# Optimization experiments

Hardware: AMD Instinct MI355X
Metric: run time of the kernel (lower is better)

The kernel has to match this reference:

```python
import jax, jax.numpy as jnp
import numpy as np

B, N, K, DIN, DM, DOUT = 4, 8192, 16, 128, 128, 128
SCALE = 1.0 / float(np.sqrt(DM))


def setup_inputs() -> dict:
    key = jax.random.key(0)
    ks = jax.random.split(key, 24)
    s = 0.05
    rnd = lambda k, shape: jax.random.normal(k, shape, jnp.float32) * s
    return {
        "relative_knn_xyz": jax.random.normal(ks[0], (B, N, K, 3), jnp.float32),
        "feature": jax.random.normal(ks[1], (B, N, DIN), jnp.float32),
        "knn_idx": jax.random.randint(ks[2], (B, N, K), 0, N),
        # fc_delta: Linear(3,DM) -> ReLU -> Linear(DM,DM)
        "Wd1": rnd(ks[3], (3, DM)), "bd1": jnp.zeros((DM,), jnp.float32),
        "Wd2": rnd(ks[4], (DM, DM)), "bd2": jnp.zeros((DM,), jnp.float32),
        # fc1: Linear(DIN, DM)
        "W1": rnd(ks[5], (DIN, DM)), "b1": jnp.zeros((DM,), jnp.float32),
        # q/k/v projections (no bias)
        "Wq": rnd(ks[6], (DM, DM)),
        "Wk": rnd(ks[7], (DM, DM)),
        "Wv": rnd(ks[8], (DM, DM)),
        # fc_gamma: Linear(DM,DM) -> ReLU -> Linear(DM,DM)
        "Wg1": rnd(ks[9], (DM, DM)), "bg1": jnp.zeros((DM,), jnp.float32),
        "Wg2": rnd(ks[10], (DM, DM)), "bg2": jnp.zeros((DM,), jnp.float32),
        # fc2: Linear(DM, DOUT)
        "W2": rnd(ks[11], (DM, DOUT)), "b2": jnp.zeros((DOUT,), jnp.float32),
        # shortout_fc: Linear(DIN, DOUT)
        "Ws": rnd(ks[12], (DIN, DOUT)), "bs": jnp.zeros((DOUT,), jnp.float32),
    }


def reference(relative_knn_xyz, feature, knn_idx,
              Wd1, bd1, Wd2, bd2, W1, b1, Wq, Wk, Wv,
              Wg1, bg1, Wg2, bg2, W2, b2, Ws, bs):
    # positional encoding of relative knn coords: [B,N,K,DM]
    pos_enc = jax.nn.relu(relative_knn_xyz @ Wd1 + bd1) @ Wd2 + bd2
    f = feature @ W1 + b1                                  # [B,N,DM]
    bidx = jnp.arange(B)[:, None, None]
    knn_f = f[bidx, knn_idx]                               # gather -> [B,N,K,DM]
    q = f @ Wq                                             # [B,N,DM]
    k = knn_f @ Wk                                         # [B,N,K,DM]
    v = knn_f @ Wv                                         # [B,N,K,DM]
    h = q[:, :, None, :] - k + pos_enc                     # [B,N,K,DM]
    logits = (jax.nn.relu(h @ Wg1 + bg1) @ Wg2 + bg2) * SCALE
    attn = jax.nn.softmax(logits, axis=-2)                 # softmax over neighbors
    agg = jnp.einsum('bnkf,bnkf->bnf', attn, v + pos_enc)  # [B,N,DM]
    return agg @ W2 + b2 + feature @ Ws + bs               # [B,N,DOUT]
```

## Files before the change

kernel.cpp:

```cpp
#include <hip/hip_runtime.h>

#define NB 4
#define NN 8192
#define NK 16
#define ND 128
#define NPTS (NB*NN)

typedef __bf16 bv8 __attribute__((ext_vector_type(8)));
typedef unsigned short us8 __attribute__((ext_vector_type(8)));
typedef float fv4 __attribute__((ext_vector_type(4)));
typedef float f32x16 __attribute__((ext_vector_type(16)));
typedef unsigned int u32;

__device__ __forceinline__ unsigned short f2b(float x){
  union { float f; unsigned u; } v; v.f = x;
  unsigned r = v.u + 0x7FFFu + ((v.u >> 16) & 1u);
  return (unsigned short)(r >> 16);
}
__device__ __forceinline__ float blo(u32 u){ return __builtin_bit_cast(float, u << 16); }
__device__ __forceinline__ float bhi(u32 u){ return __builtin_bit_cast(float, u & 0xffff0000u); }
__device__ __forceinline__ u32 pkbf(float lo, float hi){
  u32 r; asm("v_cvt_pk_bf16_f32 %0, %1, %2" : "=v"(r) : "v"(lo), "v"(hi)); return r;
}
__device__ __forceinline__ unsigned swz(int row, int cbyte){
  return (unsigned)(row*256 + (cbyte ^ ((row & 7) << 4)));
}
__device__ __forceinline__ unsigned aggoff(int pt, int c16){
  return (unsigned)(pt*128 + (c16 ^ ((pt & 7) << 3)));
}
__device__ __forceinline__ fv4 mfma16(us8 a, us8 b, fv4 c){
  return __builtin_amdgcn_mfma_f32_16x16x32_bf16(
      __builtin_bit_cast(bv8, a), __builtin_bit_cast(bv8, b), c, 0, 0, 0);
}
__device__ __forceinline__ f32x16 mfma32(us8 a, us8 b, f32x16 c){
  return __builtin_amdgcn_mfma_f32_32x32x16_bf16(
      __builtin_bit_cast(bv8, a), __builtin_bit_cast(bv8, b), c, 0, 0, 0);
}
__device__ __forceinline__ us8 mkb(u32 w0, u32 w1, u32 w2, u32 w3){
  union { u32 w[4]; us8 v; } u; u.w[0]=w0; u.w[1]=w1; u.w[2]=w2; u.w[3]=w3; return u.v;
}
__device__ __forceinline__ f32x16 zf(){
  f32x16 z;
  #pragma unroll
  for (int i=0;i<16;++i) z[i]=0.f;
  return z;
}
__device__ __forceinline__ float rsum16(float v){
  v += __builtin_bit_cast(float, __builtin_amdgcn_update_dpp(0, __builtin_bit_cast(int, v), 0x128, 0xf, 0xf, false));
  v += __builtin_bit_cast(float, __builtin_amdgcn_update_dpp(0, __builtin_bit_cast(int, v), 0x124, 0xf, 0xf, false));
  v += __builtin_bit_cast(float, __builtin_amdgcn_update_dpp(0, __builtin_bit_cast(int, v), 0x122, 0xf, 0xf, false));
  v += __builtin_bit_cast(float, __builtin_amdgcn_update_dpp(0, __builtin_bit_cast(int, v), 0x121, 0xf, 0xf, false));
  return v;
}

__global__ void pt_prep1(const float* __restrict__ Wk, const float* __restrict__ Wq,
                         const float* __restrict__ Wg1, float* __restrict__ T1, float* __restrict__ T2){
  int b = blockIdx.x;
  const float* A = (b >= 4) ? Wq : Wk;
  float* D = (b >= 4) ? T2 : T1;
  int row = (b & 3)*32 + (threadIdx.x >> 3);
  int c0 = (threadIdx.x & 7)*16;
  float acc[16];
  #pragma unroll
  for (int j=0;j<16;++j) acc[j]=0.f;
  for (int k=0;k<128;++k){
    float a = A[row*128+k];
    const float* g = Wg1 + k*128 + c0;
    #pragma unroll
    for (int j=0;j<16;++j) acc[j] = fmaf(a, g[j], acc[j]);
  }
  #pragma unroll
  for (int j=0;j<16;++j) D[row*128 + c0 + j] = acc[j];
}

__global__ void pt_prep2(const float* __restrict__ W1, const float* __restrict__ Wv,
                         const float* __restrict__ Wd2, const float* __restrict__ Wg1,
                         const float* __restrict__ T1, const float* __restrict__ T2,
                         const float* __restrict__ b1, const float* __restrict__ bd2,
                         const float* __restrict__ bg1, const float* __restrict__ b2,
                         const float* __restrict__ W2,
                         float* __restrict__ WKG, float* __restrict__ WQG,
                         float* __restrict__ WV, float* __restrict__ W21,
                         float* __restrict__ bKG, float* __restrict__ bQG,
                         float* __restrict__ bV, float* __restrict__ b2p)
{
  int b = blockIdx.x;
  if (b < 16){
    int pr = b >> 2;
    const float* A  = (pr==3) ? Wd2 : W1;
    const float* Bm = (pr==0) ? T1 : (pr==1) ? T2 : (pr==2) ? Wv : Wg1;
    float* D        = (pr==0) ? WKG : (pr==1) ? WQG : (pr==2) ? WV : W21;
    int row = (b & 3)*32 + (threadIdx.x >> 3);
    int c0 = (threadIdx.x & 7)*16;
    float acc[16];
    #pragma unroll
    for (int j=0;j<16;++j) acc[j]=0.f;
    for (int k=0;k<128;++k){
      float a = A[row*128+k];
      const float* g = Bm + k*128 + c0;
      #pragma unroll
      for (int j=0;j<16;++j) acc[j] = fmaf(a, g[j], acc[j]);
    }
    #pragma unroll
    for (int j=0;j<16;++j) D[row*128 + c0 + j] = acc[j];
  } else if (threadIdx.x < 128){
    int j = threadIdx.x;
    float s1=0.f, s2=0.f, s3=0.f, s4=0.f;
    for (int k=0;k<128;++k){
      s1 = fmaf(b1[k],  T1[k*128+j],  s1);
      s2 = fmaf(b1[k],  T2[k*128+j],  s2);
      s2 = fmaf(bd2[k], Wg1[k*128+j], s2);
      s3 = fmaf(b1[k],  Wv[k*128+j],  s3);
      s4 = fmaf(bd2[k], W2[k*128+j],  s4);
    }
    bKG[j] = s1;
    bQG[j] = s2 + bg1[j];
    bV[j]  = s3;
    b2p[j] = b2[j] + s4;
  }
}

__global__ void pt_pack(const float* __restrict__ WKG, const float* __restrict__ WQG,
                        const float* __restrict__ WV, const float* __restrict__ Ws,
                        const float* __restrict__ W21, const float* __restrict__ Wd2,
                        const float* __restrict__ Wg2, const float* __restrict__ W2,
                        const float* __restrict__ Wd1, const float* __restrict__ bd1,
                        unsigned short* __restrict__ pstd, unsigned short* __restrict__ pT,
                        unsigned short* __restrict__ pD1)
{
  int b = blockIdx.x;
  if (b < 4){
    const float* srcs[4] = {WKG, WQG, WV, Ws};
    const float* src = srcs[b];
    unsigned short* dst = pstd + b*16384;
    for (int e = threadIdx.x; e < 16384; e += blockDim.x){
      int j = e&7, lane = (e>>3)&63, ct = (e>>9)&7, kb = (e>>12)&3;
      int row = kb*32 + ((lane>>4)<<3) + j;
      int col = ct*16 + (lane&15);
      dst[e] = f2b(src[row*128+col]);
    }
  } else if (b < 8){
    const float* srcs[4] = {W21, Wd2, Wg2, W2};
    const float* src = srcs[b-4];
    unsigned short* dst = pT + (b-4)*16384;
    for (int e = threadIdx.x; e < 16384; e += blockDim.x){
      int j = e&7, lane = (e>>3)&63, kb = (e>>9)&7, mt = (e>>12)&3;
      int row = mt*32 + (lane&31);
      int k = kb*16 + ((lane>>5)<<3) + j;
      dst[e] = f2b(src[k*128+row]);
    }
  } else {
    for (int e = threadIdx.x; e < 2048; e += blockDim.x){
      int j = e&7, lane = (e>>3)&63, mt = (e>>9)&3;
      int c = mt*32 + (lane&31);
      int k = ((lane>>5)<<3) + j;
      float v = (k<3) ? Wd1[k*128+c] : ((k==3) ? bd1[c] : 0.f);
      pD1[e] = f2b(v);
    }
  }
}

__global__ __launch_bounds__(256) void pt_proj(
    const float* __restrict__ feat, const unsigned short* __restrict__ pstd,
    const float* __restrict__ bKG, const float* __restrict__ bQG,
    const float* __restrict__ bV, const float* __restrict__ bs,
    unsigned short* __restrict__ KG, unsigned short* __restrict__ QG,
    unsigned short* __restrict__ Vv, float* __restrict__ SH)
{
  __shared__ alignas(16) char ldsF[32768];
  int tid = threadIdx.x;
  int bid = blockIdx.x;
  int panel = bid & 3;
  int rb = (bid >> 2) * 128;
  {
    int rr = tid>>1, c0 = (tid&1)*64;
    const float* src = feat + (rb+rr)*128 + c0;
    #pragma unroll
    for (int c=0;c<64;c+=4){
      float4 v = *(const float4*)(src + c);
      u32 w0 = (u32)f2b(v.x) | ((u32)f2b(v.y)<<16);
      u32 w1 = (u32)f2b(v.z) | ((u32)f2b(v.w)<<16);
      *(uint2*)(ldsF + swz(rr, (c0+c)*2)) = make_uint2(w0,w1);
    }
  }
  __syncthreads();
  int w = tid>>6, l = tid&63;
  int row0 = w*32;
  int arow = l&15, acb = (l>>4)<<4;
  int crw = (l>>4)<<2, ccol = l&15;
  const unsigned short* Bp = pstd + panel*16384;
  fv4 acc[2][8];
  #pragma unroll
  for (int rt=0;rt<2;++rt)
    #pragma unroll
    for (int ct=0;ct<8;++ct) acc[rt][ct] = fv4{0.f,0.f,0.f,0.f};
  #pragma unroll
  for (int kb=0;kb<4;++kb){
    us8 a0 = *(const us8*)(ldsF + swz(row0+arow,    kb*64+acb));
    us8 a1 = *(const us8*)(ldsF + swz(row0+16+arow, kb*64+acb));
    #pragma unroll
    for (int ct=0;ct<8;++ct){
      us8 bf = *(const us8*)(Bp + ((kb*8+ct)*64 + l)*8);
      acc[0][ct] = mfma16(a0, bf, acc[0][ct]);
      acc[1][ct] = mfma16(a1, bf, acc[1][ct]);
    }
  }
  const float* bias = (panel==0)?bKG:(panel==1)?bQG:(panel==2)?bV:bs;
  if (panel < 3){
    unsigned short* dst = (panel==0)?KG:(panel==1)?QG:Vv;
    #pragma unroll
    for (int rt=0;rt<2;++rt)
      #pragma unroll
      for (int ct=0;ct<8;++ct)
        #pragma unroll
        for (int rg=0;rg<4;++rg){
          int r = row0 + rt*16 + crw + rg, c = ct*16 + ccol;
          dst[(rb+r)*128 + c] = f2b(acc[rt][ct][rg] + bias[c]);
        }
  } else {
    #pragma unroll
    for (int rt=0;rt<2;++rt)
      #pragma unroll
      for (int ct=0;ct<8;++ct)
        #pragma unroll
        for (int rg=0;rg<4;++rg){
          int r = row0 + rt*16 + crw + rg, c = ct*16 + ccol;
          SH[(rb+r)*128 + c] = acc[rt][ct][rg] + bias[c];
        }
  }
}

__global__ __launch_bounds__(512, 2) void pt_main(
    const int* __restrict__ knn, const float* __restrict__ xyz,
    const unsigned short* __restrict__ KG, const unsigned short* __restrict__ QG,
    const unsigned short* __restrict__ Vv, const float* __restrict__ SH,
    const unsigned short* __restrict__ pT, const unsigned short* __restrict__ pD1,
    const float* __restrict__ b2p, float* __restrict__ outp)
{
  __shared__ unsigned short aggL[32*128];
  const unsigned short* pW21T = pT + 0*16384;
  const unsigned short* pWd2T = pT + 1*16384;
  const unsigned short* pWg2T = pT + 2*16384;
  const unsigned short* pW2T  = pT + 3*16384;

  int tid = threadIdx.x;
  int bid = blockIdx.x;
  int wgx = (bid & 7)*256 + (bid >> 3);
  int gp0 = wgx * 16;
  int bb  = gp0 >> 13;
  int w = tid >> 6, l = tid & 63;
  int h = l >> 5, r = l & 31, p = r >> 4, n = r & 15;
  int mypt = gp0 + w*2 + p;
  int ptl  = w*2 + p;

  ((unsigned long long*)aggL)[512 + tid] = 0ull;

  int gidx = (bb << 13) + knn[mypt*16 + n];
  const float* xr = xyz + (mypt*16 + n)*3;
  float xx = xr[0], xy = xr[1], xz = xr[2];

  u32 bx0 = h ? 0u : pkbf(xx, xy);
  u32 bx1 = h ? 0u : pkbf(xz, 1.0f);
  us8 bX = mkb(bx0, bx1, 0u, 0u);
  f32x16 P1f[4];
  #pragma unroll
  for (int mt=0; mt<4; ++mt){
    us8 aW = *(const us8*)(pD1 + (mt*64 + l)*8);
    P1f[mt] = mfma32(aW, bX, zf());
  }
  u32 pw[4][4][2];
  #pragma unroll
  for (int mt=0; mt<4; ++mt)
    #pragma unroll
    for (int q=0; q<4; ++q)
      #pragma unroll
      for (int wi=0; wi<2; ++wi)
        pw[mt][q][wi] = pkbf(fmaxf(0.f, P1f[mt][4*q+2*wi]),
                             fmaxf(0.f, P1f[mt][4*q+2*wi+1]));

  u32 Bp[8][4];
  #pragma unroll
  for (int kb=0; kb<8; ++kb){
    int ms = kb>>1, qA = 2*(kb&1), qB = qA+1;
    u32 sA0 = __shfl_xor(pw[ms][qA][0], 32), sA1 = __shfl_xor(pw[ms][qA][1], 32);
    u32 sB0 = __shfl_xor(pw[ms][qB][0], 32), sB1 = __shfl_xor(pw[ms][qB][1], 32);
    Bp[kb][0] = h ? sB0 : pw[ms][qA][0];
    Bp[kb][1] = h ? sB1 : pw[ms][qA][1];
    Bp[kb][2] = h ? pw[ms][qB][0] : sA0;
    Bp[kb][3] = h ? pw[ms][qB][1] : sA1;
  }

  uint2 kg[4][4], qg[4][4];
  {
    const unsigned short* kgr = KG + gidx*128;
    const unsigned short* qgr = QG + mypt*128;
    #pragma unroll
    for (int mt=0; mt<4; ++mt)
      #pragma unroll
      for (int q=0; q<4; ++q){
        kg[mt][q] = *(const uint2*)(kgr + 32*mt + 8*q + 4*h);
        qg[mt][q] = *(const uint2*)(qgr + 32*mt + 8*q + 4*h);
      }
  }

  f32x16 pg[4];
  #pragma unroll
  for (int mt=0; mt<4; ++mt) pg[mt] = zf();
  #pragma unroll
  for (int kb=0; kb<8; ++kb){
    us8 bfr = mkb(Bp[kb][0], Bp[kb][1], Bp[kb][2], Bp[kb][3]);
    #pragma unroll
    for (int mt=0; mt<4; ++mt){
      us8 a = *(const us8*)(pW21T + ((mt*8+kb)*64 + l)*8);
      pg[mt] = mfma32(a, bfr, pg[mt]);
    }
  }

  u32 gw[4][4][2];
  #pragma unroll
  for (int mt=0; mt<4; ++mt)
    #pragma unroll
    for (int q=0; q<4; ++q){
      float g0 = fmaxf(0.f, pg[mt][4*q+0] + (blo(qg[mt][q].x) - blo(kg[mt][q].x)));
      float g1 = fmaxf(0.f, pg[mt][4*q+1] + (bhi(qg[mt][q].x) - bhi(kg[mt][q].x)));
      float g2 = fmaxf(0.f, pg[mt][4*q+2] + (blo(qg[mt][q].y) - blo(kg[mt][q].y)));
      float g3 = fmaxf(0.f, pg[mt][4*q+3] + (bhi(qg[mt][q].y) - bhi(kg[mt][q].y)));
      gw[mt][q][0] = pkbf(g0, g1);
      gw[mt][q][1] = pkbf(g2, g3);
    }
  u32 Bg[8][4];
  #pragma unroll
  for (int kb=0; kb<8; ++kb){
    int ms = kb>>1, qA = 2*(kb&1), qB = qA+1;
    u32 sA0 = __shfl_xor(gw[ms][qA][0], 32), sA1 = __shfl_xor(gw[ms][qA][1], 32);
    u32 sB0 = __shfl_xor(gw[ms][qB][0], 32), sB1 = __shfl_xor(gw[ms][qB][1], 32);
    Bg[kb][0] = h ? sB0 : gw[ms][qA][0];
    Bg[kb][1] = h ? sB1 : gw[ms][qA][1];
    Bg[kb][2] = h ? gw[ms][qB][0] : sA0;
    Bg[kb][3] = h ? gw[ms][qB][1] : sA1;
  }

  uint2 vv[4][4];
  {
    const unsigned short* vr = Vv + gidx*128;
    #pragma unroll
    for (int mt=0; mt<4; ++mt)
      #pragma unroll
      for (int q=0; q<4; ++q)
        vv[mt][q] = *(const uint2*)(vr + 32*mt + 8*q + 4*h);
  }

  f32x16 lg[4];
  #pragma unroll
  for (int mt=0; mt<4; ++mt) lg[mt] = zf();
  #pragma unroll
  for (int kb=0; kb<8; ++kb){
    us8 bfr = mkb(Bg[kb][0], Bg[kb][1], Bg[kb][2], Bg[kb][3]);
    #pragma unroll
    for (int mt=0; mt<4; ++mt){
      us8 a = *(const us8*)(pWg2T + ((mt*8+kb)*64 + l)*8);
      lg[mt] = mfma32(a, bfr, lg[mt]);
    }
  }

  const float SC = 0.08838834764831843f;
  #pragma unroll
  for (int mt=0; mt<4; ++mt){
    f32x16 ps = zf();
    #pragma unroll
    for (int kb=0; kb<8; ++kb){
      us8 a = *(const us8*)(pWd2T + ((mt*8+kb)*64 + l)*8);
      ps = mfma32(a, mkb(Bp[kb][0], Bp[kb][1], Bp[kb][2], Bp[kb][3]), ps);
    }
    float aggv[16];
    #pragma unroll
    for (int q=0; q<4; ++q){
      float wv0 = blo(vv[mt][q].x) + ps[4*q+0];
      float wv1 = bhi(vv[mt][q].x) + ps[4*q+1];
      float wv2 = blo(vv[mt][q].y) + ps[4*q+2];
      float wv3 = bhi(vv[mt][q].y) + ps[4*q+3];
      float e0 = __expf(lg[mt][4*q+0]*SC);
      float e1 = __expf(lg[mt][4*q+1]*SC);
      float e2 = __expf(lg[mt][4*q+2]*SC);
      float e3 = __expf(lg[mt][4*q+3]*SC);
      float s0 = rsum16(e0), s1 = rsum16(e1), s2 = rsum16(e2), s3 = rsum16(e3);
      float m0 = rsum16(e0*wv0), m1 = rsum16(e1*wv1), m2 = rsum16(e2*wv2), m3 = rsum16(e3*wv3);
      aggv[4*q+0] = m0 * __builtin_amdgcn_rcpf(s0);
      aggv[4*q+1] = m1 * __builtin_amdgcn_rcpf(s1);
      aggv[4*q+2] = m2 * __builtin_amdgcn_rcpf(s2);
      aggv[4*q+3] = m3 * __builtin_amdgcn_rcpf(s3);
    }
    if ((l & 15) == 15){
      #pragma unroll
      for (int q=0; q<4; ++q){
        u32 w0 = pkbf(aggv[4*q+0], aggv[4*q+1]);
        u32 w1 = pkbf(aggv[4*q+2], aggv[4*q+3]);
        *(uint2*)(aggL + aggoff(ptl, 32*mt + 8*q + 4*h)) = make_uint2(w0, w1);
      }
    }
  }
  __syncthreads();

  if (w < 4){
    int mt = w;
    f32x16 o = zf();
    #pragma unroll
    for (int kb=0; kb<8; ++kb){
      us8 a = *(const us8*)(pW2T + ((mt*8+kb)*64 + l)*8);
      us8 bfr = *(const us8*)(aggL + aggoff(l&31, kb*16 + 8*h));
      o = mfma32(a, bfr, o);
    }
    int pt = l & 31;
    if (pt < 16){
      float* orow = outp + (gp0 + pt)*128;
      const float* shrow = SH + (gp0 + pt)*128;
      #pragma unroll
      for (int q=0; q<4; ++q){
        int cb = 32*mt + 8*q + 4*h;
        float4 b4 = *(const float4*)(b2p + cb);
        float4 s4 = *(const float4*)(shrow + cb);
        float4 res;
        res.x = o[4*q+0] + b4.x + s4.x;
        res.y = o[4*q+1] + b4.y + s4.y;
        res.z = o[4*q+2] + b4.z + s4.z;
        res.w = o[4*q+3] + b4.w + s4.w;
        *(float4*)(orow + cb) = res;
      }
    }
  }
}

extern "C" void kernel_launch(void* const* d_in, const int* in_sizes, int n_in,
                              void* d_out, int out_size, void* d_ws, size_t ws_size,
                              hipStream_t stream)
{
  const float* xyz     = (const float*)d_in[0];
  const float* feature = (const float*)d_in[1];
  const int*   knn     = (const int*)d_in[2];
  const float* Wd1 = (const float*)d_in[3];
  const float* bd1 = (const float*)d_in[4];
  const float* Wd2 = (const float*)d_in[5];
  const float* bd2 = (const float*)d_in[6];
  const float* W1  = (const float*)d_in[7];
  const float* b1  = (const float*)d_in[8];
  const float* Wq  = (const float*)d_in[9];
  const float* Wk  = (const float*)d_in[10];
  const float* Wv  = (const float*)d_in[11];
  const float* Wg1 = (const float*)d_in[12];
  const float* bg1 = (const float*)d_in[13];
  const float* Wg2 = (const float*)d_in[14];
  const float* bg2 = (const float*)d_in[15];
  const float* W2  = (const float*)d_in[16];
  const float* b2  = (const float*)d_in[17];
  const float* Ws  = (const float*)d_in[18];
  const float* bs  = (const float*)d_in[19];
  (void)bg2;

  char* ws = (char*)d_ws;
  unsigned short* KGa  = (unsigned short*)(ws + 0);
  unsigned short* QGa  = (unsigned short*)(ws + 8388608);
  unsigned short* Va   = (unsigned short*)(ws + 16777216);
  float*          SHa  = (float*)(ws + 25165824);
  unsigned short* PSTD = (unsigned short*)(ws + 41943040);
  unsigned short* PT   = (unsigned short*)(ws + 42074112);
  unsigned short* PD1  = (unsigned short*)(ws + 42205184);
  float* T1   = (float*)(ws + 42209280);
  float* T2   = (float*)(ws + 42274816);
  float* WKGf = (float*)(ws + 42340352);
  float* WQGf = (float*)(ws + 42405888);
  float* WVf  = (float*)(ws + 42471424);
  float* W21f = (float*)(ws + 42536960);
  float* bKG  = (float*)(ws + 42602496);
  float* bQG  = (float*)(ws + 42603008);
  float* bV   = (float*)(ws + 42603520);
  float* b2p  = (float*)(ws + 42604032);

  pt_prep1<<<8, 256, 0, stream>>>(Wk, Wq, Wg1, T1, T2);
  pt_prep2<<<17, 256, 0, stream>>>(W1, Wv, Wd2, Wg1, T1, T2, b1, bd2, bg1, b2, W2,
                                   WKGf, WQGf, WVf, W21f, bKG, bQG, bV, b2p);
  pt_pack<<<9, 256, 0, stream>>>(WKGf, WQGf, WVf, Ws, W21f, Wd2, Wg2, W2, Wd1, bd1,
                                 PSTD, PT, PD1);
  pt_proj<<<1024, 256, 0, stream>>>(feature, PSTD, bKG, bQG, bV, bs, KGa, QGa, Va, SHa);
  pt_main<<<2048, 512, 0, stream>>>(knn, xyz, KGa, QGa, Va, SHa, PT, PD1, b2p, (float*)d_out);
}
```

Measured before the change: 363.1 us.

## Fold q/k/v row adds into MFMA via identity matrices and use permlane32 swaps

The q-minus-k and v row additions move into the MFMA accumulators through extra MFMAs with ±identity A operands, in place of per-element bf16 unpacking and scalar adds. Gathered rows are loaded as 16-byte vectors, and the half-wave shuffles become v_permlane32_swap. The softmax scale and log2(e) are folded into Wg2 at pack time so exp2 can be used directly, and the small prep GEMMs are register-tiled with float4 loads. This adds MFMA work and identity-operand registers in exchange for fewer VALU and shuffle instructions.

Measured after the change: 306.5 us. 15.6% less time.

```diff
diff --git a/kernel.cpp b/kernel.cpp
--- a/kernel.cpp
+++ b/kernel.cpp
@@ -17,8 +17,6 @@
   unsigned r = v.u + 0x7FFFu + ((v.u >> 16) & 1u);
   return (unsigned short)(r >> 16);
 }
-__device__ __forceinline__ float blo(u32 u){ return __builtin_bit_cast(float, u << 16); }
-__device__ __forceinline__ float bhi(u32 u){ return __builtin_bit_cast(float, u & 0xffff0000u); }
 __device__ __forceinline__ u32 pkbf(float lo, float hi){
   u32 r; asm("v_cvt_pk_bf16_f32 %0, %1, %2" : "=v"(r) : "v"(lo), "v"(hi)); return r;
 }
@@ -52,25 +50,39 @@
   v += __builtin_bit_cast(float, __builtin_amdgcn_update_dpp(0, __builtin_bit_cast(int, v), 0x121, 0xf, 0xf, false));
   return v;
 }
+__device__ __forceinline__ void plswap(u32& a, u32& b){
+  asm("v_permlane32_swap_b32 %0, %1" : "+v"(a), "+v"(b));
+}
 
 __global__ void pt_prep1(const float* __restrict__ Wk, const float* __restrict__ Wq,
                          const float* __restrict__ Wg1, float* __restrict__ T1, float* __restrict__ T2){
   int b = blockIdx.x;
   const float* A = (b >= 4) ? Wq : Wk;
   float* D = (b >= 4) ? T2 : T1;
-  int row = (b & 3)*32 + (threadIdx.x >> 3);
-  int c0 = (threadIdx.x & 7)*16;
-  float acc[16];
-  #pragma unroll
-  for (int j=0;j<16;++j) acc[j]=0.f;
-  for (int k=0;k<128;++k){
-    float a = A[row*128+k];
-    const float* g = Wg1 + k*128 + c0;
-    #pragma unroll
-    for (int j=0;j<16;++j) acc[j] = fmaf(a, g[j], acc[j]);
-  }
-  #pragma unroll
-  for (int j=0;j<16;++j) D[row*128 + c0 + j] = acc[j];
+  int r0 = (b & 3)*32 + (threadIdx.x >> 5)*4;
+  int c0 = (threadIdx.x & 31)*4;
+  float4 acc[4];
+  #pragma unroll
+  for (int i=0;i<4;++i) acc[i] = make_float4(0.f,0.f,0.f,0.f);
+  for (int k = 0; k < 128; k += 4){
+    float4 a[4];
+    #pragma unroll
+    for (int i=0;i<4;++i) a[i] = *(const float4*)(A + (r0+i)*128 + k);
+    #pragma unroll
+    for (int kk=0; kk<4; ++kk){
+      float4 bv = *(const float4*)(Wg1 + (k+kk)*128 + c0);
+      #pragma unroll
+      for (int i=0;i<4;++i){
+        float av = (kk==0)?a[i].x:(kk==1)?a[i].y:(kk==2)?a[i].z:a[i].w;
+        acc[i].x = fmaf(av, bv.x, acc[i].x);
+        acc[i].y = fmaf(av, bv.y, acc[i].y);
+        acc[i].z = fmaf(av, bv.z, acc[i].z);
+        acc[i].w = fmaf(av, bv.w, acc[i].w);
+      }
+    }
+  }
+  #pragma unroll
+  for (int i=0;i<4;++i) *(float4*)(D + (r0+i)*128 + c0) = acc[i];
 }
 
 __global__ void pt_prep2(const float* __restrict__ W1, const float* __restrict__ Wv,
@@ -90,19 +102,30 @@
     const float* A  = (pr==3) ? Wd2 : W1;
     const float* Bm = (pr==0) ? T1 : (pr==1) ? T2 : (pr==2) ? Wv : Wg1;
     float* D        = (pr==0) ? WKG : (pr==1) ? WQG : (pr==2) ? WV : W21;
-    int row = (b & 3)*32 + (threadIdx.x >> 3);
-    int c0 = (threadIdx.x & 7)*16;
-    float acc[16];
-    #pragma unroll
-    for (int j=0;j<16;++j) acc[j]=0.f;
-    for (int k=0;k<128;++k){
-      float a = A[row*128+k];
-      const float* g = Bm + k*128 + c0;
-      #pragma unroll
-      for (int j=0;j<16;++j) acc[j] = fmaf(a, g[j], acc[j]);
-    }
-    #pragma unroll
-    for (int j=0;j<16;++j) D[row*128 + c0 + j] = acc[j];
+    int r0 = (b & 3)*32 + (threadIdx.x >> 5)*4;
+    int c0 = (threadIdx.x & 31)*4;
+    float4 acc[4];
+    #pragma unroll
+    for (int i=0;i<4;++i) acc[i] = make_float4(0.f,0.f,0.f,0.f);
+    for (int k = 0; k < 128; k += 4){
+      float4 a[4];
+      #pragma unroll
+      for (int i=0;i<4;++i) a[i] = *(const float4*)(A + (r0+i)*128 + k);
+      #pragma unroll
+      for (int kk=0; kk<4; ++kk){
+        float4 bv = *(const float4*)(Bm + (k+kk)*128 + c0);
+        #pragma unroll
+        for (int i=0;i<4;++i){
+          float av = (kk==0)?a[i].x:(kk==1)?a[i].y:(kk==2)?a[i].z:a[i].w;
+          acc[i].x = fmaf(av, bv.x, acc[i].x);
+          acc[i].y = fmaf(av, bv.y, acc[i].y);
+          acc[i].z = fmaf(av, bv.z, acc[i].z);
+          acc[i].w = fmaf(av, bv.w, acc[i].w);
+        }
+      }
+    }
+    #pragma unroll
+    for (int i=0;i<4;++i) *(float4*)(D + (r0+i)*128 + c0) = acc[i];
   } else if (threadIdx.x < 128){
     int j = threadIdx.x;
     float s1=0.f, s2=0.f, s3=0.f, s4=0.f;
@@ -142,12 +165,13 @@
   } else if (b < 8){
     const float* srcs[4] = {W21, Wd2, Wg2, W2};
     const float* src = srcs[b-4];
+    float scale = (b==6) ? 0.127517445f : 1.0f;
     unsigned short* dst = pT + (b-4)*16384;
     for (int e = threadIdx.x; e < 16384; e += blockDim.x){
       int j = e&7, lane = (e>>3)&63, kb = (e>>9)&7, mt = (e>>12)&3;
       int row = mt*32 + (lane&31);
       int k = kb*16 + ((lane>>5)<<3) + j;
-      dst[e] = f2b(src[k*128+row]);
+      dst[e] = f2b(src[k*128+row] * scale);
     }
   } else {
     for (int e = threadIdx.x; e < 2048; e += blockDim.x){
@@ -259,6 +283,21 @@
   const float* xr = xyz + (mypt*16 + n)*3;
   float xx = xr[0], xy = xr[1], xz = xr[2];
 
+  int rl = r, hh = h;
+  u32 ip0[4], ip1[4], in0[4], in1[4];
+  #pragma unroll
+  for (int wj=0; wj<4; ++wj){
+    int k0 = 8*hh + 2*wj, k1 = k0 + 1;
+    ip0[wj] = (rl==k0 ? 0x3F80u : 0u) | (rl==k1 ? 0x3F800000u : 0u);
+    in0[wj] = (rl==k0 ? 0xBF80u : 0u) | (rl==k1 ? 0xBF800000u : 0u);
+    ip1[wj] = (rl==16+k0 ? 0x3F80u : 0u) | (rl==16+k1 ? 0x3F800000u : 0u);
+    in1[wj] = (rl==16+k0 ? 0xBF80u : 0u) | (rl==16+k1 ? 0xBF800000u : 0u);
+  }
+  us8 Ip0 = mkb(ip0[0],ip0[1],ip0[2],ip0[3]);
+  us8 Ip1 = mkb(ip1[0],ip1[1],ip1[2],ip1[3]);
+  us8 In0 = mkb(in0[0],in0[1],in0[2],in0[3]);
+  us8 In1 = mkb(in1[0],in1[1],in1[2],in1[3]);
+
   u32 bx0 = h ? 0u : pkbf(xx, xy);
   u32 bx1 = h ? 0u : pkbf(xz, 1.0f);
   us8 bX = mkb(bx0, bx1, 0u, 0u);
@@ -282,38 +321,33 @@
   #pragma unroll
   for (int kb=0; kb<8; ++kb){
     int ms = kb>>1, qA = 2*(kb&1), qB = qA+1;
-    u32 sA0 = __shfl_xor(pw[ms][qA][0], 32), sA1 = __shfl_xor(pw[ms][qA][1], 32);
-    u32 sB0 = __shfl_xor(pw[ms][qB][0], 32), sB1 = __shfl_xor(pw[ms][qB][1], 32);
-    Bp[kb][0] = h ? sB0 : pw[ms][qA][0];
-    Bp[kb][1] = h ? sB1 : pw[ms][qA][1];
-    Bp[kb][2] = h ? pw[ms][qB][0] : sA0;
-    Bp[kb][3] = h ? pw[ms][qB][1] : sA1;
-  }
-
-  uint2 kg[4][4], qg[4][4];
-  {
-    const unsigned short* kgr = KG + gidx*128;
-    const unsigned short* qgr = QG + mypt*128;
-    #pragma unroll
-    for (int mt=0; mt<4; ++mt)
-      #pragma unroll
-      for (int q=0; q<4; ++q){
-        kg[mt][q] = *(const uint2*)(kgr + 32*mt + 8*q + 4*h);
-        qg[mt][q] = *(const uint2*)(qgr + 32*mt + 8*q + 4*h);
-      }
-  }
-
+    u32 a0 = pw[ms][qA][0], b0 = pw[ms][qB][0];
+    u32 a1 = pw[ms][qA][1], b1 = pw[ms][qB][1];
+    plswap(a0, b0);
+    plswap(a1, b1);
+    Bp[kb][0] = a0; Bp[kb][1] = a1; Bp[kb][2] = b0; Bp[kb][3] = b1;
+  }
+
+  const unsigned short* qrowb = QG + (long)mypt*ND + 8*h;
+  const unsigned short* krowb = KG + (long)gidx*ND + 8*h;
   f32x16 pg[4];
   #pragma unroll
-  for (int mt=0; mt<4; ++mt) pg[mt] = zf();
-  #pragma unroll
-  for (int kb=0; kb<8; ++kb){
-    us8 bfr = mkb(Bp[kb][0], Bp[kb][1], Bp[kb][2], Bp[kb][3]);
-    #pragma unroll
-    for (int mt=0; mt<4; ++mt){
+  for (int mt=0; mt<4; ++mt){
+    us8 q0 = *(const us8*)(qrowb + 32*mt);
+    us8 q1 = *(const us8*)(qrowb + 32*mt + 16);
+    us8 k0 = *(const us8*)(krowb + 32*mt);
+    us8 k1 = *(const us8*)(krowb + 32*mt + 16);
+    f32x16 acc = zf();
+    #pragma unroll
+    for (int kb=0; kb<8; ++kb){
       us8 a = *(const us8*)(pW21T + ((mt*8+kb)*64 + l)*8);
-      pg[mt] = mfma32(a, bfr, pg[mt]);
-    }
+      acc = mfma32(a, mkb(Bp[kb][0], Bp[kb][1], Bp[kb][2], Bp[kb][3]), acc);
+    }
+    acc = mfma32(Ip0, q0, acc);
+    acc = mfma32(Ip1, q1, acc);
+    acc = mfma32(In0, k0, acc);
+    acc = mfma32(In1, k1, acc);
+    pg[mt] = acc;
   }
 
   u32 gw[4][4][2];
@@ -321,33 +355,18 @@
   for (int mt=0; mt<4; ++mt)
     #pragma unroll
     for (int q=0; q<4; ++q){
-      float g0 = fmaxf(0.f, pg[mt][4*q+0] + (blo(qg[mt][q].x) - blo(kg[mt][q].x)));
-      float g1 = fmaxf(0.f, pg[mt][4*q+1] + (bhi(qg[mt][q].x) - bhi(kg[mt][q].x)));
-      float g2 = fmaxf(0.f, pg[mt][4*q+2] + (blo(qg[mt][q].y) - blo(kg[mt][q].y)));
-      float g3 = fmaxf(0.f, pg[mt][4*q+3] + (bhi(qg[mt][q].y) - bhi(kg[mt][q].y)));
-      gw[mt][q][0] = pkbf(g0, g1);
-      gw[mt][q][1] = pkbf(g2, g3);
+      gw[mt][q][0] = pkbf(fmaxf(0.f, pg[mt][4*q+0]), fmaxf(0.f, pg[mt][4*q+1]));
+      gw[mt][q][1] = pkbf(fmaxf(0.f, pg[mt][4*q+2]), fmaxf(0.f, pg[mt][4*q+3]));
     }
   u32 Bg[8][4];
   #pragma unroll
   for (int kb=0; kb<8; ++kb){
     int ms = kb>>1, qA = 2*(kb&1), qB = qA+1;
-    u32 sA0 = __shfl_xor(gw[ms][qA][0], 32), sA1 = __shfl_xor(gw[ms][qA][1], 32);
-    u32 sB0 = __shfl_xor(gw[ms][qB][0], 32), sB1 = __shfl_xor(gw[ms][qB][1], 32);
-    Bg[kb][0] = h ? sB0 : gw[ms][qA][0];
-    Bg[kb][1] = h ? sB1 : gw[ms][qA][1];
-    Bg[kb][2] = h ? gw[ms][qB][0] : sA0;
-    Bg[kb][3] = h ? gw[ms][qB][1] : sA1;
-  }
-
-  uint2 vv[4][4];
-  {
-    const unsigned short* vr = Vv + gidx*128;
-    #pragma unroll
-    for (int mt=0; mt<4; ++mt)
-      #pragma unroll
-      for (int q=0; q<4; ++q)
-        vv[mt][q] = *(const uint2*)(vr + 32*mt + 8*q + 4*h);
+    u32 a0 = gw[ms][qA][0], b0 = gw[ms][qB][0];
+    u32 a1 = gw[ms][qA][1], b1 = gw[ms][qB][1];
+    plswap(a0, b0);
+    plswap(a1, b1);
+    Bg[kb][0] = a0; Bg[kb][1] = a1; Bg[kb][2] = b0; Bg[kb][3] = b1;
   }
 
   f32x16 lg[4];
@@ -363,7 +382,9 @@
     }
   }
 
-  const float SC = 0.08838834764831843f;
+  const unsigned short* vrowb = Vv + (long)gidx*ND + 8*h;
+  us8 v0 = *(const us8*)(vrowb);
+  us8 v1 = *(const us8*)(vrowb + 16);
   #pragma unroll
   for (int mt=0; mt<4; ++mt){
     f32x16 ps = zf();
@@ -372,19 +393,22 @@
       us8 a = *(const us8*)(pWd2T + ((mt*8+kb)*64 + l)*8);
       ps = mfma32(a, mkb(Bp[kb][0], Bp[kb][1], Bp[kb][2], Bp[kb][3]), ps);
     }
+    ps = mfma32(Ip0, v0, ps);
+    ps = mfma32(Ip1, v1, ps);
+    if (mt < 3){
+      v0 = *(const us8*)(vrowb + 32*(mt+1));
+      v1 = *(const us8*)(vrowb + 32*(mt+1) + 16);
+    }
     float aggv[16];
     #pragma unroll
     for (int q=0; q<4; ++q){
-      float wv0 = blo(vv[mt][q].x) + ps[4*q+0];
-      float wv1 = bhi(vv[mt][q].x) + ps[4*q+1];
-      float wv2 = blo(vv[mt][q].y) + ps[4*q+2];
-      float wv3 = bhi(vv[mt][q].y) + ps[4*q+3];
-      float e0 = __expf(lg[mt][4*q+0]*SC);
-      float e1 = __expf(lg[mt][4*q+1]*SC);
-      float e2 = __expf(lg[mt][4*q+2]*SC);
-      float e3 = __expf(lg[mt][4*q+3]*SC);
+      float e0 = exp2f(lg[mt][4*q+0]);
+      float e1 = exp2f(lg[mt][4*q+1]);
+      float e2 = exp2f(lg[mt][4*q+2]);
+      float e3 = exp2f(lg[mt][4*q+3]);
       float s0 = rsum16(e0), s1 = rsum16(e1), s2 = rsum16(e2), s3 = rsum16(e3);
-      float m0 = rsum16(e0*wv0), m1 = rsum16(e1*wv1), m2 = rsum16(e2*wv2), m3 = rsum16(e3*wv3);
+      float m0 = rsum16(e0*ps[4*q+0]), m1 = rsum16(e1*ps[4*q+1]);
+      float m2 = rsum16(e2*ps[4*q+2]), m3 = rsum16(e3*ps[4*q+3]);
       aggv[4*q+0] = m0 * __builtin_amdgcn_rcpf(s0);
       aggv[4*q+1] = m1 * __builtin_amdgcn_rcpf(s1);
       aggv[4*q+2] = m2 * __builtin_amdgcn_rcpf(s2);
```
